# Optimization experiments

Hardware: AMD Instinct MI355X
Metric: run time of the kernel (lower is better)

Reference implementation:

```python
import jax, jax.numpy as jnp
import numpy as np

DIM = 384
NUM_HEADS = 12
HEAD_DIM = 32
MID = NUM_HEADS * HEAD_DIM
RES = (32, 32)


def _relative_position_index(res):
    Hh, Ww = res
    coords = np.stack(np.meshgrid(np.arange(Hh), np.arange(Ww), indexing='ij'))  # 2,H,W
    cf = coords.reshape(2, -1)
    rel = cf[:, :, None] - cf[:, None, :]  # 2,N,N
    rel = rel.transpose(1, 2, 0).astype(np.int64)
    rel[:, :, 0] += Hh - 1
    rel[:, :, 1] += Ww - 1
    rel[:, :, 0] *= 2 * Ww - 1
    return rel.sum(-1)  # N,N


def setup_inputs() -> dict:
    key = jax.random.key(0)
    ks = jax.random.split(key, 8)
    B = 8
    Hh, Ww = RES
    table_size = (2 * Hh - 1) * (2 * Ww - 1)
    x = jax.random.normal(ks[0], (B, DIM, Hh, Ww), dtype=jnp.float32)
    wq = jax.random.normal(ks[1], (MID, DIM), dtype=jnp.float32) * 0.02
    bq = jnp.zeros((MID,), dtype=jnp.float32)
    wkv = jax.random.normal(ks[2], (2 * MID, DIM), dtype=jnp.float32) * 0.02
    bkv = jnp.zeros((2 * MID,), dtype=jnp.float32)
    wproj = jax.random.normal(ks[3], (DIM, MID), dtype=jnp.float32) * 0.02
    bproj = jnp.zeros((DIM,), dtype=jnp.float32)
    bias_table = jax.random.normal(ks[4], (table_size, NUM_HEADS), dtype=jnp.float32) * 0.02
    rel_index = jnp.asarray(_relative_position_index(RES), dtype=jnp.int32)  # N,N
    return {"x": x, "wq": wq, "bq": bq, "wkv": wkv, "bkv": bkv,
            "wproj": wproj, "bproj": bproj, "bias_table": bias_table,
            "rel_index": rel_index}


def reference(x, wq, bq, wkv, bkv, wproj, bproj, bias_table, rel_index):
    B, C, Hh, Ww = x.shape
    N = Hh * Ww
    scale = HEAD_DIM ** -0.5
    xf = x.reshape(B, C, N)  # B,C,N
    # 1x1 convs == channelwise linear
    q = jnp.einsum('oc,bcn->bon', wq, xf) + bq[None, :, None]          # B,MID,N
    kv = jnp.einsum('oc,bcn->bon', wkv, xf) + bkv[None, :, None]       # B,2*MID,N
    q = q.reshape(B, NUM_HEADS, HEAD_DIM, N).transpose(0, 1, 3, 2)     # B,h,N,d
    kv = kv.reshape(B, 2, NUM_HEADS, HEAD_DIM, N)
    k = kv[:, 0].transpose(0, 1, 3, 2)                                  # B,h,N,d
    v = kv[:, 1].transpose(0, 1, 3, 2)                                  # B,h,N,d
    attn = jnp.einsum('bhnd,bhmd->bhnm', q, k) * scale                  # B,h,N,N
    rel_bias = bias_table[rel_index.reshape(-1)].reshape(N, N, NUM_HEADS)
    attn = attn + rel_bias.transpose(2, 0, 1)[None]                     # + h,N,N bias
    attn = jax.nn.softmax(attn, axis=-1)
    out = jnp.einsum('bhnm,bhmd->bhnd', attn, v)                        # B,h,N,d
    out = out.transpose(0, 1, 3, 2).reshape(B, MID, N)                  # B,MID,N
    out = jnp.einsum('om,bmn->bon', wproj, out) + bproj[None, :, None]  # B,DIM,N
    return out.reshape(B, C, Hh, Ww)
```

## Files before the change

kernel.cpp:

```cpp
#include <hip/hip_runtime.h>

typedef __bf16 bf16;
typedef __bf16 bf16x8 __attribute__((ext_vector_type(8)));
typedef __bf16 bf16x4 __attribute__((ext_vector_type(4)));
typedef float  f32x4  __attribute__((ext_vector_type(4)));

static constexpr int NB = 8;
static constexpr int NH = 12;
static constexpr int HD = 32;
static constexpr int NN = 1024;
static constexpr int NC = 384;

static constexpr float LOG2E = 1.4426950408889634f;
static constexpr float QSC   = (float)(0.17677669529663687 * 1.4426950408889634);

static constexpr size_t XT_N   = (size_t)NB*NN*NC;
static constexpr size_t WQKV_N = (size_t)3*NC*NC;
static constexpr size_t WP_N   = (size_t)NC*NC;
static constexpr size_t QKV_N  = (size_t)NB*NH*NN*HD;
static constexpr size_t AO_N   = (size_t)NB*NN*NC;

static constexpr size_t XT_OFF   = 0;
static constexpr size_t WQKV_OFF = XT_OFF + XT_N;
static constexpr size_t WP_OFF   = WQKV_OFF + WQKV_N;
static constexpr size_t Q_OFF    = WP_OFF + WP_N;
static constexpr size_t K_OFF    = Q_OFF + QKV_N;
static constexpr size_t V_OFF    = K_OFF + QKV_N;
static constexpr size_t AO_OFF   = V_OFF + QKV_N;
static constexpr size_t PT_OFF   = AO_OFF + AO_N;

static constexpr int PT_PER_H = 63 * 62;
static constexpr int PT_TOTAL = NH * PT_PER_H;

#define MFMA16(a,b,c) __builtin_amdgcn_mfma_f32_16x16x32_bf16(a,b,c,0,0,0)

static __device__ inline float fast_exp2(float x) {
#if __has_builtin(__builtin_amdgcn_exp2f)
    return __builtin_amdgcn_exp2f(x);
#else
    return exp2f(x);
#endif
}

__global__ __launch_bounds__(256) void cast_all_kernel(const float* __restrict__ x,
                                                       const float* __restrict__ wq,
                                                       const float* __restrict__ wkv,
                                                       const float* __restrict__ wproj,
                                                       const float* __restrict__ bias_table,
                                                       bf16* __restrict__ xt,
                                                       bf16* __restrict__ wqkv,
                                                       bf16* __restrict__ wp,
                                                       unsigned* __restrict__ PT)
{
    __shared__ bf16 T[64][68];
    const int t = threadIdx.x;
    if (blockIdx.x >= 1344) {
        const int e = (blockIdx.x - 1344) * 256 + t;
        if (e >= PT_TOTAL) return;
        const int h = e / PT_PER_H, rem = e - h * PT_PER_H;
        const int dj = rem / 62, dip = rem - dj * 62;
        bf16 lo = (bf16)(bias_table[(size_t)((dip + 1) * 63 + dj) * NH + h] * LOG2E);
        bf16 hi = (bf16)(bias_table[(size_t)(dip * 63 + dj) * NH + h] * LOG2E);
        PT[e] = (unsigned)__builtin_bit_cast(unsigned short, lo)
              | ((unsigned)__builtin_bit_cast(unsigned short, hi) << 16);
        return;
    }
    if (blockIdx.x >= 768) {
        const size_t i = ((size_t)(blockIdx.x - 768) * 256 + t) * 4;
        if (i >= WQKV_N + WP_N) return;
        const float* src; bf16* dst;
        if (i < (size_t)NC*NC)      { src = wq + i;                     dst = wqkv + i; }
        else if (i < WQKV_N)        { src = wkv + (i - (size_t)NC*NC);  dst = wqkv + i; }
        else                        { src = wproj + (i - WQKV_N);       dst = wp + (i - WQKV_N); }
        float4 v = *(const float4*)src;
        bf16x4 o; o[0] = (bf16)v.x; o[1] = (bf16)v.y; o[2] = (bf16)v.z; o[3] = (bf16)v.w;
        *(bf16x4*)dst = o;
        return;
    }
    const int bid = blockIdx.x;
    const int b = bid / 96, rem = bid % 96, ct = rem >> 4, nt = rem & 15;
    const int c0 = ct * 64, n0 = nt * 64;
    const float* Xb = x + (size_t)b * NC * NN;
    const int nl = t & 63, c4 = (t >> 6) * 4;
#pragma unroll
    for (int i = 0; i < 4; ++i) {
        const int c = c4 + i * 16;
        bf16x4 v;
#pragma unroll
        for (int j = 0; j < 4; ++j)
            v[j] = (bf16)Xb[(size_t)(c0 + c + j) * NN + n0 + nl];
        *(bf16x4*)&T[nl][c] = v;
    }
    __syncthreads();
    const int n = t >> 2;
#pragma unroll
    for (int i = 0; i < 2; ++i) {
        const int cg = (t & 3) * 8 + i * 32;
        bf16x4 a = *(const bf16x4*)&T[n][cg];
        bf16x4 bv = *(const bf16x4*)&T[n][cg + 4];
        bf16x8 vv = __builtin_shufflevector(a, bv, 0, 1, 2, 3, 4, 5, 6, 7);
        *(bf16x8*)&xt[((size_t)b * NN + n0 + n) * NC + c0 + cg] = vv;
    }
}

__global__ __launch_bounds__(256) void qkv_gemm_kernel(
    const bf16* __restrict__ W, const bf16* __restrict__ Xt,
    const float* __restrict__ bq, const float* __restrict__ bkv,
    bf16* __restrict__ Qd, bf16* __restrict__ Kd, bf16* __restrict__ Vd)
{
    __shared__ bf16 As[128][72];
    __shared__ bf16 Bs[128][72];
    const int t = threadIdx.x;
    const int w = t >> 6, lane = t & 63, g = lane >> 4, l16 = lane & 15;
    const int wm = w >> 1, wn = w & 1;
    const int n0g = blockIdx.x * 128;
    const int b = n0g >> 10, n0 = n0g & 1023;
    const int o0 = blockIdx.y * 128;
    const bf16* Xb = Xt + (size_t)b * NN * NC;

    const int sr = t >> 1, sc2 = (t & 1) * 32;

    f32x4 acc[4][4] = {};

    bf16x8 aw[4], bw[4];
#pragma unroll
    for (int i = 0; i < 4; ++i) {
        aw[i] = *(const bf16x8*)&W [(size_t)(o0 + sr) * NC + sc2 + 8*i];
        bw[i] = *(const bf16x8*)&Xb[(size_t)(n0 + sr) * NC + sc2 + 8*i];
    }

    for (int k0 = 0; k0 < NC; k0 += 64) {
        __syncthreads();
#pragma unroll
        for (int i = 0; i < 4; ++i) {
            *(bf16x8*)&As[sr][sc2 + 8*i] = aw[i];
            *(bf16x8*)&Bs[sr][sc2 + 8*i] = bw[i];
        }
        __syncthreads();
        if (k0 + 64 < NC) {
#pragma unroll
            for (int i = 0; i < 4; ++i) {
                aw[i] = *(const bf16x8*)&W [(size_t)(o0 + sr) * NC + k0 + 64 + sc2 + 8*i];
                bw[i] = *(const bf16x8*)&Xb[(size_t)(n0 + sr) * NC + k0 + 64 + sc2 + 8*i];
            }
        }
#pragma unroll
        for (int ks = 0; ks < 2; ++ks) {
            bf16x8 a[4], bb[4];
#pragma unroll
            for (int s = 0; s < 4; ++s) {
                a[s]  = *(const bf16x8*)&As[wm*64 + s*16 + l16][ks*32 + g*8];
                bb[s] = *(const bf16x8*)&Bs[wn*64 + s*16 + l16][ks*32 + g*8];
            }
#pragma unroll
            for (int sm = 0; sm < 4; ++sm)
#pragma unroll
                for (int sn = 0; sn < 4; ++sn)
                    acc[sm][sn] = MFMA16(a[sm], bb[sn], acc[sm][sn]);
        }
    }

#pragma unroll
    for (int sm = 0; sm < 4; ++sm)
#pragma unroll
    for (int sn = 0; sn < 4; ++sn) {
        const int col   = n0 + wn*64 + sn*16 + l16;
        const int obase = o0 + wm*64 + sm*16 + g*4;
        f32x4 v = acc[sm][sn];
        if (obase < 384) {
            const int hh = obase >> 5, d = obase & 31;
            bf16x4 o4;
#pragma unroll
            for (int r = 0; r < 4; ++r) o4[r] = (bf16)((v[r] + bq[obase + r]) * QSC);
            *(bf16x4*)&Qd[(((size_t)b*NH + hh)*NN + col)*HD + d] = o4;
        } else if (obase < 768) {
            const int oo = obase - 384; const int hh = oo >> 5, d = oo & 31;
            bf16x4 o4;
#pragma unroll
            for (int r = 0; r < 4; ++r) o4[r] = (bf16)(v[r] + bkv[oo + r]);
            *(bf16x4*)&Kd[(((size_t)b*NH + hh)*NN + col)*HD + d] = o4;
        } else {
            const int oo = obase - 768; const int hh = oo >> 5, d = oo & 31;
#pragma unroll
            for (int r = 0; r < 4; ++r)
                Vd[(((size_t)b*NH + hh)*HD + d + r)*NN + col] = (bf16)(v[r] + bkv[obase - 384 + r]);
        }
    }
}

__global__ __launch_bounds__(512, 3) void attn_kernel(
    const bf16* __restrict__ Qg, const bf16* __restrict__ Kg, const bf16* __restrict__ Vg,
    const unsigned* __restrict__ PT, bf16* __restrict__ AOt)
{
    __shared__ __align__(16) char arena[47488];
    bf16 (*KsH)[128][40]   = (bf16 (*)[128][40])arena;
    bf16 (*VsH)[2][32][72] = (bf16 (*)[2][32][72])(arena + 20480);
    unsigned (*pairTw)[34] = (unsigned (*)[34])(arena + 38912);

    const int t = threadIdx.x;
    const int w = t >> 6, lane = t & 63, g = lane >> 4, l16 = lane & 15;
    const int wl = w & 3, hf = w >> 2;

    const int bid = blockIdx.x;
    const int nid = (bid & 7) * 96 + (bid >> 3);
    const int qt = nid & 7;
    const int hb = nid >> 3;
    const int h = hb % 12, b = hb / 12;

    const bf16* Qb = Qg + ((size_t)(b*NH + h)) * NN * HD;
    const bf16* Kb = Kg + ((size_t)(b*NH + h)) * NN * HD;
    const bf16* Vb = Vg + ((size_t)(b*NH + h)) * HD * NN;

    const int tl = t & 255, g2 = t >> 8;
    const int kr = tl >> 1, kc2 = (tl & 1) * 16;
    const int vd = tl >> 3, vmb = (tl & 7) * 16;
    int vsub[2], vqa[2];
#pragma unroll
    for (int i = 0; i < 2; ++i) {
        const int vm = vmb + 8*i, vmm = vm & 63;
        vsub[i] = vm >> 6;
        vqa[i]  = ((vmm >> 5) & 1) * 32 + ((vmm >> 2) & 3) * 8 + ((vmm >> 4) & 1) * 4;
    }
    const int mbase = g2 * 512;

    bf16x8 sregK[2], sregV[2];
#pragma unroll
    for (int i = 0; i < 2; ++i) {
        sregK[i] = *(const bf16x8*)&Kb[(size_t)(mbase + kr) * HD + kc2 + 8*i];
        sregV[i] = *(const bf16x8*)&Vb[(size_t)vd * NN + mbase + vmb + 8*i];
    }

    const int q0 = qt * 128;
    const bf16x8 qfrag0 = *(const bf16x8*)&Qb[(size_t)(q0 + wl*32      + l16) * HD + g*8];
    const bf16x8 qfrag1 = *(const bf16x8*)&Qb[(size_t)(q0 + wl*32 + 16 + l16) * HD + g*8];

    const unsigned* PTh = PT + (size_t)h * PT_PER_H + 4 * qt;
    for (int idx = t; idx < 63 * 34; idx += 512) {
        const int dj = idx / 34, dipl = idx - dj * 34;
        pairTw[dj][dipl] = PTh[dj * 62 + dipl];
    }

    const unsigned* twp = &pairTw[0][0];
    const int rowD1 = (l16 + 31 - 4*g) * 34;

    bf16x8 vones;
#pragma unroll
    for (int e = 0; e < 8; ++e) vones[e] = (bf16)1.0f;

    f32x4 oacc0[2] = {}, oacc1[2] = {};
    f32x4 oacc_l0 = {}, oacc_l1 = {};

    for (int ph = 0; ph < 4; ++ph) {
        __syncthreads();
#pragma unroll
        for (int i = 0; i < 2; ++i) {
            *(bf16x8*)&KsH[g2][kr][kc2 + 8*i] = sregK[i];
            bf16x4 vlo = __builtin_shufflevector(sregV[i], sregV[i], 0, 1, 2, 3);
            bf16x4 vhi = __builtin_shufflevector(sregV[i], sregV[i], 4, 5, 6, 7);
            *(bf16x4*)&VsH[g2][vsub[i]][vd][vqa[i]]     = vlo;
            *(bf16x4*)&VsH[g2][vsub[i]][vd][vqa[i] + 8] = vhi;
        }
        __syncthreads();
        if (ph < 3) {
            const int m1 = mbase + (ph + 1) * 128;
#pragma unroll
            for (int i = 0; i < 2; ++i) {
                sregK[i] = *(const bf16x8*)&Kb[(size_t)(m1 + kr) * HD + kc2 + 8*i];
                sregV[i] = *(const bf16x8*)&Vb[(size_t)vd * NN + m1 + vmb + 8*i];
            }
        }

#pragma unroll
        for (int sub = 0; sub < 2; ++sub) {
            const int it = hf * 8 + 2 * ph + sub;
            const bf16 (*Vsp)[72] = VsH[hf][sub];
            const int dipl = wl + 30 - 2*it;
            const unsigned* pD1 = twp + rowD1 + dipl;

            f32x4 b00, b01, b02, b03, b10, b12;
#pragma unroll
            for (int r = 0; r < 4; ++r) {
                const unsigned d1w = pD1[-34 * r];
                const unsigned d0w = pD1[-34 * r - 544];
                const unsigned d2w = pD1[-34 * r + 544];
                b00[r] = __uint_as_float(d1w << 16);
                b02[r] = __uint_as_float(d1w & 0xFFFF0000u);
                b01[r] = __uint_as_float(d0w << 16);
                b03[r] = __uint_as_float(d0w & 0xFFFF0000u);
                b10[r] = __uint_as_float(d2w << 16);
                b12[r] = __uint_as_float(d2w & 0xFFFF0000u);
            }
            f32x4 bacc0[4] = {b00, b01, b02, b03};
            f32x4 bacc1[4] = {b10, b00, b12, b02};

            bf16x8 pa0[2], pa1[2];
#pragma unroll
            for (int sc = 0; sc < 4; ++sc) {
                bf16x8 kf = *(const bf16x8*)&KsH[hf][sub*64 + sc*16 + l16][g*8];
                f32x4 z0 = MFMA16(kf, qfrag0, bacc0[sc]);
                f32x4 z1 = MFMA16(kf, qfrag1, bacc1[sc]);
                const int kc = sc >> 1, hl = (sc & 1) * 4;
#pragma unroll
                for (int r = 0; r < 4; ++r) {
                    pa0[kc][hl + r] = (bf16)fast_exp2(z0[r]);
                    pa1[kc][hl + r] = (bf16)fast_exp2(z1[r]);
                }
            }

#pragma unroll
            for (int kc = 0; kc < 2; ++kc) {
#pragma unroll
                for (int ds = 0; ds < 2; ++ds) {
                    bf16x8 vf = *(const bf16x8*)&Vsp[ds*16 + l16][kc*32 + 8*g];
                    oacc0[ds] = MFMA16(pa0[kc], vf, oacc0[ds]);
                    oacc1[ds] = MFMA16(pa1[kc], vf, oacc1[ds]);
                }
                oacc_l0 = MFMA16(pa0[kc], vones, oacc_l0);
                oacc_l1 = MFMA16(pa1[kc], vones, oacc_l1);
            }
        }
    }

    __syncthreads();
    f32x4* mbuf = (f32x4*)arena;
    const int sb = wl * 64 + lane;
    if (hf == 1) {
        mbuf[0*256 + sb] = oacc0[0]; mbuf[1*256 + sb] = oacc0[1];
        mbuf[2*256 + sb] = oacc1[0]; mbuf[3*256 + sb] = oacc1[1];
        mbuf[4*256 + sb] = oacc_l0;  mbuf[5*256 + sb] = oacc_l1;
    }
    __syncthreads();
    if (hf == 0) {
        oacc0[0] += mbuf[0*256 + sb]; oacc0[1] += mbuf[1*256 + sb];
        oacc1[0] += mbuf[2*256 + sb]; oacc1[1] += mbuf[3*256 + sb];
        oacc_l0  += mbuf[4*256 + sb]; oacc_l1  += mbuf[5*256 + sb];

        float rin0[4], rin1[4];
#pragma unroll
        for (int r = 0; r < 4; ++r) {
            rin0[r] = 1.0f / oacc_l0[r];
            rin1[r] = 1.0f / oacc_l1[r];
        }
        const int nrow0 = q0 + wl*32 + g*4;
#pragma unroll
        for (int ds = 0; ds < 2; ++ds) {
            const int c = h*HD + ds*16 + l16;
#pragma unroll
            for (int r = 0; r < 4; ++r) {
                AOt[((size_t)b*NN + nrow0 + r)      * NC + c] = (bf16)(oacc0[ds][r] * rin0[r]);
                AOt[((size_t)b*NN + nrow0 + 16 + r) * NC + c] = (bf16)(oacc1[ds][r] * rin1[r]);
            }
        }
    }
}

__global__ __launch_bounds__(256) void proj_gemm_kernel(
    const bf16* __restrict__ W, const bf16* __restrict__ AOt,
    const float* __restrict__ bproj, float* __restrict__ out)
{
    __shared__ bf16 As[64][40];
    __shared__ bf16 Bs[128][40];
    const int t = threadIdx.x;
    const int w = t >> 6, lane = t & 63, g = lane >> 4, l16 = lane & 15;
    const int wm = w >> 1, wn = w & 1;
    const int n0g = blockIdx.x * 128;
    const int b = n0g >> 10, n0 = n0g & 1023;
    const int o0 = blockIdx.y * 64;
    const bf16* Ab = AOt + (size_t)b * NN * NC;

    const int ar = t >> 2, ac = (t & 3) * 8;

    f32x4 acc[2][4] = {};

    bf16x8 aw = *(const bf16x8*)&W[(size_t)(o0 + ar) * NC + ac];
    bf16x8 bw[2];
#pragma unroll
    for (int i = 0; i < 2; ++i) {
        const int s = t + i * 256, r = s >> 2, cc = (s & 3) * 8;
        bw[i] = *(const bf16x8*)&Ab[(size_t)(n0 + r) * NC + cc];
    }

    for (int k0 = 0; k0 < NC; k0 += 32) {
        __syncthreads();
        *(bf16x8*)&As[ar][ac] = aw;
#pragma unroll
        for (int i = 0; i < 2; ++i) {
            const int s = t + i * 256, r = s >> 2, cc = (s & 3) * 8;
            *(bf16x8*)&Bs[r][cc] = bw[i];
        }
        __syncthreads();
        if (k0 + 32 < NC) {
            aw = *(const bf16x8*)&W[(size_t)(o0 + ar) * NC + k0 + 32 + ac];
#pragma unroll
            for (int i = 0; i < 2; ++i) {
                const int s = t + i * 256, r = s >> 2, cc = (s & 3) * 8;
                bw[i] = *(const bf16x8*)&Ab[(size_t)(n0 + r) * NC + k0 + 32 + cc];
            }
        }
        bf16x8 a0 = *(const bf16x8*)&As[wm*32      + l16][g*8];
        bf16x8 a1 = *(const bf16x8*)&As[wm*32 + 16 + l16][g*8];
#pragma unroll
        for (int sn = 0; sn < 4; ++sn) {
            bf16x8 bf = *(const bf16x8*)&Bs[wn*64 + sn*16 + l16][g*8];
            acc[0][sn] = MFMA16(a0, bf, acc[0][sn]);
            acc[1][sn] = MFMA16(a1, bf, acc[1][sn]);
        }
    }

#pragma unroll
    for (int sm = 0; sm < 2; ++sm)
#pragma unroll
    for (int sn = 0; sn < 4; ++sn) {
        const int col   = n0 + wn*64 + sn*16 + l16;
        const int obase = o0 + wm*32 + sm*16 + g*4;
        f32x4 v = acc[sm][sn];
#pragma unroll
        for (int r = 0; r < 4; ++r)
            out[((size_t)b*NC + obase + r)*NN + col] = v[r] + bproj[obase + r];
    }
}

extern "C" void kernel_launch(void* const* d_in, const int* in_sizes, int n_in,
                              void* d_out, int out_size, void* d_ws, size_t ws_size,
                              hipStream_t stream)
{
    const float* x          = (const float*)d_in[0];
    const float* wq         = (const float*)d_in[1];
    const float* bq         = (const float*)d_in[2];
    const float* wkv        = (const float*)d_in[3];
    const float* bkv        = (const float*)d_in[4];
    const float* wproj      = (const float*)d_in[5];
    const float* bproj      = (const float*)d_in[6];
    const float* bias_table = (const float*)d_in[7];
    float* out = (float*)d_out;

    bf16* wsb  = (bf16*)d_ws;
    bf16* Xt   = wsb + XT_OFF;
    bf16* Wqkv = wsb + WQKV_OFF;
    bf16* Wp   = wsb + WP_OFF;
    bf16* Qd   = wsb + Q_OFF;
    bf16* Kd   = wsb + K_OFF;
    bf16* Vd   = wsb + V_OFF;
    bf16* AOt  = wsb + AO_OFF;
    unsigned* PT = (unsigned*)(wsb + PT_OFF);

    const int ptBlocks = (PT_TOTAL + 255) / 256;
    cast_all_kernel<<<dim3(768 + 576 + ptBlocks), 256, 0, stream>>>(
        x, wq, wkv, wproj, bias_table, Xt, Wqkv, Wp, PT);
    qkv_gemm_kernel<<<dim3(64, 9), 256, 0, stream>>>(Wqkv, Xt, bq, bkv, Qd, Kd, Vd);
    attn_kernel<<<dim3(768), 512, 0, stream>>>(Qd, Kd, Vd, PT, AOt);
    proj_gemm_kernel<<<dim3(64, 6), 256, 0, stream>>>(Wp, AOt, bproj, out);
}
```

Measured before the change: 63.76 us.

## Fuse fp32 input/weight cast and transpose into QKV GEMM tile loads

Removes the separate cast/transpose pass over x and the QKV weights. The QKV GEMM now reads fp32 x and weights directly, converts them to bf16 and transposes while staging into shared memory. This avoids writing and re-reading a bf16 copy of x. The launch also becomes 1D with an XCD-aware block remap that groups output tiles sharing the same n-tile. In exchange the GEMM loads twice as many bytes per tile and does the conversion work redundantly across the 9 output tiles. Its transposed shared-memory stores may also cause bank conflicts.

```diff
diff --git a/kernel.cpp b/kernel.cpp
--- a/kernel.cpp
+++ b/kernel.cpp
@@ -14,15 +14,11 @@
 static constexpr float LOG2E = 1.4426950408889634f;
 static constexpr float QSC   = (float)(0.17677669529663687 * 1.4426950408889634);
 
-static constexpr size_t XT_N   = (size_t)NB*NN*NC;
-static constexpr size_t WQKV_N = (size_t)3*NC*NC;
 static constexpr size_t WP_N   = (size_t)NC*NC;
 static constexpr size_t QKV_N  = (size_t)NB*NH*NN*HD;
 static constexpr size_t AO_N   = (size_t)NB*NN*NC;
 
-static constexpr size_t XT_OFF   = 0;
-static constexpr size_t WQKV_OFF = XT_OFF + XT_N;
-static constexpr size_t WP_OFF   = WQKV_OFF + WQKV_N;
+static constexpr size_t WP_OFF   = 0;
 static constexpr size_t Q_OFF    = WP_OFF + WP_N;
 static constexpr size_t K_OFF    = Q_OFF + QKV_N;
 static constexpr size_t V_OFF    = K_OFF + QKV_N;
@@ -42,69 +38,33 @@
 #endif
 }
 
-__global__ __launch_bounds__(256) void cast_all_kernel(const float* __restrict__ x,
-                                                       const float* __restrict__ wq,
-                                                       const float* __restrict__ wkv,
-                                                       const float* __restrict__ wproj,
-                                                       const float* __restrict__ bias_table,
-                                                       bf16* __restrict__ xt,
-                                                       bf16* __restrict__ wqkv,
-                                                       bf16* __restrict__ wp,
-                                                       unsigned* __restrict__ PT)
+__global__ __launch_bounds__(256) void cast_pt_kernel(const float* __restrict__ wproj,
+                                                      const float* __restrict__ bias_table,
+                                                      bf16* __restrict__ wp,
+                                                      unsigned* __restrict__ PT)
 {
-    __shared__ bf16 T[64][68];
     const int t = threadIdx.x;
-    if (blockIdx.x >= 1344) {
-        const int e = (blockIdx.x - 1344) * 256 + t;
-        if (e >= PT_TOTAL) return;
-        const int h = e / PT_PER_H, rem = e - h * PT_PER_H;
-        const int dj = rem / 62, dip = rem - dj * 62;
-        bf16 lo = (bf16)(bias_table[(size_t)((dip + 1) * 63 + dj) * NH + h] * LOG2E);
-        bf16 hi = (bf16)(bias_table[(size_t)(dip * 63 + dj) * NH + h] * LOG2E);
-        PT[e] = (unsigned)__builtin_bit_cast(unsigned short, lo)
-              | ((unsigned)__builtin_bit_cast(unsigned short, hi) << 16);
+    if (blockIdx.x < 144) {
+        const size_t i = ((size_t)blockIdx.x * 256 + t) * 4;
+        if (i >= WP_N) return;
+        float4 v = *(const float4*)(wproj + i);
+        bf16x4 o; o[0] = (bf16)v.x; o[1] = (bf16)v.y; o[2] = (bf16)v.z; o[3] = (bf16)v.w;
+        *(bf16x4*)(wp + i) = o;
         return;
     }
-    if (blockIdx.x >= 768) {
-        const size_t i = ((size_t)(blockIdx.x - 768) * 256 + t) * 4;
-        if (i >= WQKV_N + WP_N) return;
-        const float* src; bf16* dst;
-        if (i < (size_t)NC*NC)      { src = wq + i;                     dst = wqkv + i; }
-        else if (i < WQKV_N)        { src = wkv + (i - (size_t)NC*NC);  dst = wqkv + i; }
-        else                        { src = wproj + (i - WQKV_N);       dst = wp + (i - WQKV_N); }
-        float4 v = *(const float4*)src;
-        bf16x4 o; o[0] = (bf16)v.x; o[1] = (bf16)v.y; o[2] = (bf16)v.z; o[3] = (bf16)v.w;
-        *(bf16x4*)dst = o;
-        return;
-    }
-    const int bid = blockIdx.x;
-    const int b = bid / 96, rem = bid % 96, ct = rem >> 4, nt = rem & 15;
-    const int c0 = ct * 64, n0 = nt * 64;
-    const float* Xb = x + (size_t)b * NC * NN;
-    const int nl = t & 63, c4 = (t >> 6) * 4;
-#pragma unroll
-    for (int i = 0; i < 4; ++i) {
-        const int c = c4 + i * 16;
-        bf16x4 v;
-#pragma unroll
-        for (int j = 0; j < 4; ++j)
-            v[j] = (bf16)Xb[(size_t)(c0 + c + j) * NN + n0 + nl];
-        *(bf16x4*)&T[nl][c] = v;
-    }
-    __syncthreads();
-    const int n = t >> 2;
-#pragma unroll
-    for (int i = 0; i < 2; ++i) {
-        const int cg = (t & 3) * 8 + i * 32;
-        bf16x4 a = *(const bf16x4*)&T[n][cg];
-        bf16x4 bv = *(const bf16x4*)&T[n][cg + 4];
-        bf16x8 vv = __builtin_shufflevector(a, bv, 0, 1, 2, 3, 4, 5, 6, 7);
-        *(bf16x8*)&xt[((size_t)b * NN + n0 + n) * NC + c0 + cg] = vv;
-    }
+    const int e = (blockIdx.x - 144) * 256 + t;
+    if (e >= PT_TOTAL) return;
+    const int h = e / PT_PER_H, rem = e - h * PT_PER_H;
+    const int dj = rem / 62, dip = rem - dj * 62;
+    bf16 lo = (bf16)(bias_table[(size_t)((dip + 1) * 63 + dj) * NH + h] * LOG2E);
+    bf16 hi = (bf16)(bias_table[(size_t)(dip * 63 + dj) * NH + h] * LOG2E);
+    PT[e] = (unsigned)__builtin_bit_cast(unsigned short, lo)
+          | ((unsigned)__builtin_bit_cast(unsigned short, hi) << 16);
 }
 
 __global__ __launch_bounds__(256) void qkv_gemm_kernel(
-    const bf16* __restrict__ W, const bf16* __restrict__ Xt,
+    const float* __restrict__ wq, const float* __restrict__ wkv,
+    const float* __restrict__ x,
     const float* __restrict__ bq, const float* __restrict__ bkv,
     bf16* __restrict__ Qd, bf16* __restrict__ Kd, bf16* __restrict__ Vd)
 {
@@ -113,36 +73,55 @@
     const int t = threadIdx.x;
     const int w = t >> 6, lane = t & 63, g = lane >> 4, l16 = lane & 15;
     const int wm = w >> 1, wn = w & 1;
-    const int n0g = blockIdx.x * 128;
+
+    const int wgid = (blockIdx.x & 7) * 72 + (blockIdx.x >> 3);
+    const int nt = wgid / 9, ot = wgid - nt * 9;
+    const int n0g = nt * 128;
     const int b = n0g >> 10, n0 = n0g & 1023;
-    const int o0 = blockIdx.y * 128;
-    const bf16* Xb = Xt + (size_t)b * NN * NC;
+    const int o0 = ot * 128;
+    const float* Wsrc = (o0 < 384) ? (wq + (size_t)o0 * NC)
+                                   : (wkv + (size_t)(o0 - 384) * NC);
+    const float* Xb = x + (size_t)b * NC * NN;
 
     const int sr = t >> 1, sc2 = (t & 1) * 32;
+    const int nq = t & 31, kg = t >> 5;
 
     f32x4 acc[4][4] = {};
 
-    bf16x8 aw[4], bw[4];
-#pragma unroll
-    for (int i = 0; i < 4; ++i) {
-        aw[i] = *(const bf16x8*)&W [(size_t)(o0 + sr) * NC + sc2 + 8*i];
-        bw[i] = *(const bf16x8*)&Xb[(size_t)(n0 + sr) * NC + sc2 + 8*i];
-    }
+    float4 af[8], bx[8];
+#pragma unroll
+    for (int u = 0; u < 8; ++u)
+        af[u] = *(const float4*)&Wsrc[(size_t)sr * NC + sc2 + 4*u];
+#pragma unroll
+    for (int j = 0; j < 8; ++j)
+        bx[j] = *(const float4*)&Xb[(size_t)(kg*8 + j) * NN + n0 + nq*4];
 
     for (int k0 = 0; k0 < NC; k0 += 64) {
         __syncthreads();
 #pragma unroll
         for (int i = 0; i < 4; ++i) {
-            *(bf16x8*)&As[sr][sc2 + 8*i] = aw[i];
-            *(bf16x8*)&Bs[sr][sc2 + 8*i] = bw[i];
+            bf16x8 v;
+            v[0] = (bf16)af[2*i].x;   v[1] = (bf16)af[2*i].y;
+            v[2] = (bf16)af[2*i].z;   v[3] = (bf16)af[2*i].w;
+            v[4] = (bf16)af[2*i+1].x; v[5] = (bf16)af[2*i+1].y;
+            v[6] = (bf16)af[2*i+1].z; v[7] = (bf16)af[2*i+1].w;
+            *(bf16x8*)&As[sr][sc2 + 8*i] = v;
+        }
+#pragma unroll
+        for (int i = 0; i < 4; ++i) {
+            bf16x8 v;
+#pragma unroll
+            for (int j = 0; j < 8; ++j) v[j] = (bf16)((&bx[j].x)[i]);
+            *(bf16x8*)&Bs[nq*4 + i][kg*8] = v;
         }
         __syncthreads();
         if (k0 + 64 < NC) {
 #pragma unroll
-            for (int i = 0; i < 4; ++i) {
-                aw[i] = *(const bf16x8*)&W [(size_t)(o0 + sr) * NC + k0 + 64 + sc2 + 8*i];
-                bw[i] = *(const bf16x8*)&Xb[(size_t)(n0 + sr) * NC + k0 + 64 + sc2 + 8*i];
-            }
+            for (int u = 0; u < 8; ++u)
+                af[u] = *(const float4*)&Wsrc[(size_t)sr * NC + k0 + 64 + sc2 + 4*u];
+#pragma unroll
+            for (int j = 0; j < 8; ++j)
+                bx[j] = *(const float4*)&Xb[(size_t)(k0 + 64 + kg*8 + j) * NN + n0 + nq*4];
         }
 #pragma unroll
         for (int ks = 0; ks < 2; ++ks) {
@@ -435,8 +414,6 @@
     float* out = (float*)d_out;
 
     bf16* wsb  = (bf16*)d_ws;
-    bf16* Xt   = wsb + XT_OFF;
-    bf16* Wqkv = wsb + WQKV_OFF;
     bf16* Wp   = wsb + WP_OFF;
     bf16* Qd   = wsb + Q_OFF;
     bf16* Kd   = wsb + K_OFF;
@@ -445,9 +422,8 @@
     unsigned* PT = (unsigned*)(wsb + PT_OFF);
 
     const int ptBlocks = (PT_TOTAL + 255) / 256;
-    cast_all_kernel<<<dim3(768 + 576 + ptBlocks), 256, 0, stream>>>(
-        x, wq, wkv, wproj, bias_table, Xt, Wqkv, Wp, PT);
-    qkv_gemm_kernel<<<dim3(64, 9), 256, 0, stream>>>(Wqkv, Xt, bq, bkv, Qd, Kd, Vd);
+    cast_pt_kernel<<<dim3(144 + ptBlocks), 256, 0, stream>>>(wproj, bias_table, Wp, PT);
+    qkv_gemm_kernel<<<dim3(576), 256, 0, stream>>>(wq, wkv, x, bq, bkv, Qd, Kd, Vd);
     attn_kernel<<<dim3(768), 512, 0, stream>>>(Qd, Kd, Vd, PT, AOt);
     proj_gemm_kernel<<<dim3(64, 6), 256, 0, stream>>>(Wp, AOt, bproj, out);
 }
```

New measurement: 80.14 us. +25.7%, slower.
